# Optimization experiments

Measured on AMD Instinct MI355X. Metric: run time of the kernel, lower is better.

The kernel has to match this reference:

```python
import jax, jax.numpy as jnp
import numpy as np


def _conv(x, w):
    # 'same'-padded NCHW conv, stride 1, no bias (matches nn.Conv2d(..., padding=k//2, bias=False))
    return jax.lax.conv_general_dilated(x, w, (1, 1), 'SAME',
                                        dimension_numbers=('NCHW', 'OIHW', 'NCHW'))


def setup_inputs() -> dict:
    key = jax.random.key(0)
    ks = jax.random.split(key, 11)
    b, C, H, W = 8, 64, 192, 192
    n_classes, n_space = 2, 8
    return {
        'x': jax.random.normal(ks[0], (b, C, H, W), jnp.float32),
        'class_score': jax.random.normal(ks[1], (b, n_classes, H, W), jnp.float32),
        # to_cspace: Conv2d(1, n_space-1, 3, padding=1)
        'W_cspace': jax.random.normal(ks[2], (n_space - 1, 1, 3, 3), jnp.float32) * 0.1,
        # to_xspace: Conv2d(C, C*n_space, 3, padding=1)
        'W_xspace': jax.random.normal(ks[3], (C * n_space, C, 3, 3), jnp.float32) * 0.02,
        # 1x1 convs stored as squeezed vectors (no bias)
        'W_combine_space': jax.random.normal(ks[4], (n_space,), jnp.float32) * 0.3,  # Conv2d(n_space,1,1)
        'W_cvalue': jax.random.normal(ks[5], (n_space,), jnp.float32) * 0.3,        # Conv2d(1,n_space,1)
        'W_attn': jax.random.normal(ks[6], (n_space,), jnp.float32) * 0.3,          # Conv2d(1,n_space,1)
        'W_combine': jax.random.normal(ks[7], (n_space,), jnp.float32) * 0.3,       # Conv2d(n_space,1,1)
        # single_conv: Conv2d(C,C,3) + BatchNorm2d(C) + ReLU
        'W_single': jax.random.normal(ks[8], (C, C, 3, 3), jnp.float32) * 0.02,
        'bn_gamma': jnp.ones((C,), jnp.float32),
        'bn_beta': jnp.zeros((C,), jnp.float32),
    }


def reference(x, class_score, W_cspace, W_xspace, W_combine_space, W_cvalue,
              W_attn, W_combine, W_single, bn_gamma, bn_beta):
    b, C, H, Wd = x.shape
    nc = class_score.shape[1]           # n_classes
    s = W_cvalue.shape[0]               # n_space
    class_prob = jax.nn.sigmoid(class_score)                       # (b, c, H, W)

    # per-class spatial 'spaces'
    space0 = class_prob.reshape(b * nc, 1, H, Wd)                  # (b*c, 1, H, W)
    space = jnp.concatenate([space0, jax.nn.sigmoid(_conv(space0, W_cspace))], axis=1)  # (b*c, s, H, W)
    space_norm = space / jnp.sum(space, axis=(2, 3), keepdims=True)
    space_norm = space_norm.reshape(b, nc, s, H, Wd).transpose(0, 2, 1, 3, 4)  # (b, s, c, H, W)

    # project x into s spaces, then contract over spatial dims (replaces broadcast-mul + double sum)
    xv = _conv(x, W_xspace).reshape(b, s, C, H, Wd)                # (b, s, d, H, W)
    tok = jnp.einsum('bsdhw,bschw->bscd', xv, space_norm)          # (b, s, c, d)
    tok = jnp.einsum('s,bscd->bcd', W_combine_space, tok)          # combine_space 1x1 conv -> (b, c, d)

    # class value / attention (1x1 convs over a singleton channel == broadcast scale)
    cval = tok[:, None] * W_cvalue[None, :, None, None]            # (b, s, c, d)
    attn = class_prob.reshape(b, nc, H * Wd).transpose(0, 2, 1)    # (b, hw, c)
    attn = jax.nn.sigmoid(attn[:, None] * W_attn[None, :, None, None])  # (b, s, hw, c)

    # attention matmul + combine 1x1 conv fused into one contraction (linear ops commute)
    info = jnp.einsum('s,bsnc,bscd->bnd', W_combine, attn, cval)   # (b, hw, d)
    info = info.transpose(0, 2, 1).reshape(b, C, H, Wd)            # (b, d, H, W)

    # single_conv: conv3x3 -> BatchNorm2d (training-mode batch stats, biased var) -> ReLU
    y = _conv(info, W_single)
    mean = jnp.mean(y, axis=(0, 2, 3), keepdims=True)
    var = jnp.var(y, axis=(0, 2, 3), keepdims=True)
    y = jax.nn.relu((y - mean) * jax.lax.rsqrt(var + 1e-5)
                    * bn_gamma[None, :, None, None] + bn_beta[None, :, None, None])
    return x + y
```

## Files before the change

### kernel.cpp

```cpp
#include <hip/hip_runtime.h>
#include <math.h>

#define B   8
#define C   64
#define HH  192
#define WWD 192
#define P   (HH*WWD)
#define NC  2
#define NS  8
#define PP  (194*194)

#define OFF_SPACE 0
#define OFF_SPART 4817408
#define OFF_R     4835840
#define OFF_TOK2  4909568
#define OFF_U     4910592
#define OFF_STP   4919808
#define OFF_SCALE 4956672
#define OFF_SHIFT 4956736
#define WS_FLOATS 4956800

__device__ __forceinline__ float sigm(float x) { return 1.0f / (1.0f + expf(-x)); }

__global__ void k_space(const float* __restrict__ cs, const float* __restrict__ Wc,
                        float* __restrict__ spp, float* __restrict__ Spart) {
    int m = blockIdx.y;
    int bx = blockIdx.x;
    int p = bx * 256 + threadIdx.x;
    int h = p / WWD, w = p - (p / WWD) * WWD;
    float cp[9];
    #pragma unroll
    for (int ky = 0; ky < 3; ky++)
        #pragma unroll
        for (int kx = 0; kx < 3; kx++) {
            int hh = h + ky - 1, ww = w + kx - 1;
            float v = 0.f;
            if ((unsigned)hh < HH && (unsigned)ww < WWD)
                v = sigm(cs[m * P + hh * WWD + ww]);
            cp[ky * 3 + kx] = v;
        }
    float ch[8];
    ch[0] = cp[4];
    #pragma unroll
    for (int j = 0; j < 7; j++) {
        float a = 0.f;
        #pragma unroll
        for (int k = 0; k < 9; k++) a += Wc[j * 9 + k] * cp[k];
        ch[j + 1] = sigm(a);
    }
    #pragma unroll
    for (int q = 0; q < 8; q++)
        spp[(m * 8 + q) * PP + (h + 1) * 194 + (w + 1)] = ch[q];
    __shared__ float red[4][8];
    int lane = threadIdx.x & 63, wave = threadIdx.x >> 6;
    #pragma unroll
    for (int q = 0; q < 8; q++) {
        float v = ch[q];
        for (int off = 32; off > 0; off >>= 1) v += __shfl_down(v, off);
        if (lane == 0) red[wave][q] = v;
    }
    __syncthreads();
    if (threadIdx.x < 8) {
        int q = threadIdx.x;
        Spart[(m * 8 + q) * 144 + bx] = red[0][q] + red[1][q] + red[2][q] + red[3][q];
    }
}

__launch_bounds__(256, 3)
__global__ void k_R2(const float* __restrict__ x, const float* __restrict__ spp,
                     float* __restrict__ R) {
    int ig = blockIdx.x;
    int scz = blockIdx.y;
    int b  = blockIdx.z;
    int sc = scz & 15;
    int half = scz >> 4;
    int s = sc >> 1, c = sc & 1;
    const float* xb = x + (b * C + ig * 8) * P;
    const float* sp = spp + ((b * NC + c) * NS + s) * PP;

    float acc[8][9];
    #pragma unroll
    for (int i = 0; i < 8; i++)
        #pragma unroll
        for (int t = 0; t < 9; t++) acc[i][t] = 0.f;

    for (int it = half * 18; it < half * 18 + 18; it++) {
        int p0 = it * 1024 + threadIdx.x * 4;
        int h = p0 / WWD, w0 = p0 - (p0 / WWD) * WWD;
        float4 xv[8];
        #pragma unroll
        for (int i = 0; i < 8; i++) xv[i] = *(const float4*)(xb + i * P + p0);
        float g[3][6];
        #pragma unroll
        for (int ty = 0; ty < 3; ty++) {
            const float* rp = sp + (h + 2 - ty) * 194 + w0;
            #pragma unroll
            for (int cc = 0; cc < 6; cc++) g[ty][cc] = rp[cc];
        }
        #pragma unroll
        for (int ty = 0; ty < 3; ty++)
            #pragma unroll
            for (int tx = 0; tx < 3; tx++) {
                float g0 = g[ty][2 - tx], g1 = g[ty][3 - tx];
                float g2 = g[ty][4 - tx], g3 = g[ty][5 - tx];
                #pragma unroll
                for (int i = 0; i < 8; i++) {
                    float a = acc[i][ty * 3 + tx];
                    a += xv[i].x * g0; a += xv[i].y * g1;
                    a += xv[i].z * g2; a += xv[i].w * g3;
                    acc[i][ty * 3 + tx] = a;
                }
            }
    }

    __shared__ float red[4][72];
    int lane = threadIdx.x & 63, wave = threadIdx.x >> 6;
    #pragma unroll
    for (int i = 0; i < 8; i++)
        #pragma unroll
        for (int t = 0; t < 9; t++) {
            float v = acc[i][t];
            for (int off = 32; off > 0; off >>= 1) v += __shfl_down(v, off);
            if (lane == 0) red[wave][i * 9 + t] = v;
        }
    __syncthreads();
    if (threadIdx.x < 72) {
        int i = threadIdx.x / 9, t = threadIdx.x - (threadIdx.x / 9) * 9;
        float v = red[0][threadIdx.x] + red[1][threadIdx.x] +
                  red[2][threadIdx.x] + red[3][threadIdx.x];
        atomicAdd(&R[((b * 16 + sc) * 64 + (ig * 8 + i)) * 9 + t], v);
    }
}

__global__ void k_tok2(const float* __restrict__ Wxs, const float* __restrict__ Wcs,
                       const float* __restrict__ R, const float* __restrict__ Spart,
                       float* __restrict__ tok2) {
    int bc = blockIdx.x, s = blockIdx.y;
    int d = threadIdx.x;
    const float* spp = Spart + (bc * 8 + s) * 144;
    float sv = 0.f;
    for (int k = d; k < 144; k += 64) sv += spp[k];
    #pragma unroll
    for (int msk = 32; msk >= 1; msk >>= 1) sv += __shfl_xor(sv, msk);

    const float* Rp = R + ((bc & 1) + ((bc >> 1) * 16 + s * 2)) * 64 * 9;
    const float* Wp = Wxs + (s * C + d) * (C * 9);
    float a = 0.f;
    for (int t = 0; t < C * 9; t++) a += Wp[t] * Rp[t];
    float val = a * Wcs[s] / sv;
    atomicAdd(&tok2[bc * C + d], val);
}

__global__ void k_U(const float* __restrict__ Ws, const float* __restrict__ tok2,
                    float* __restrict__ U) {
    int b = blockIdx.x, m = blockIdx.y, oc = threadIdx.x;
    const float* tp = tok2 + (b * NC + m) * C;
    float u[9];
    #pragma unroll
    for (int t = 0; t < 9; t++) u[t] = 0.f;
    for (int ci = 0; ci < C; ci++) {
        float tv = tp[ci];
        const float* wp = Ws + (oc * C + ci) * 9;
        #pragma unroll
        for (int t = 0; t < 9; t++) u[t] += wp[t] * tv;
    }
    float* up = U + ((b * C + oc) * 2 + m) * 9;
    #pragma unroll
    for (int t = 0; t < 9; t++) up[t] = u[t];
}

__device__ __forceinline__ void stage_g(const float* __restrict__ cs, int b, int ty0, int tx0,
                                        const float* __restrict__ Wcval,
                                        const float* __restrict__ Wattn,
                                        const float* __restrict__ Wcomb,
                                        float* h0, float* h1) {
    float wa[8], wt[8];
    #pragma unroll
    for (int s = 0; s < 8; s++) { wa[s] = Wcomb[s] * Wcval[s]; wt[s] = Wattn[s]; }
    for (int idx = threadIdx.x; idx < 34 * 34; idx += 256) {
        int i = idx / 34, j = idx - (idx / 34) * 34;
        int gy = ty0 - 1 + i, gx = tx0 - 1 + j;
        float a0 = 0.f, a1 = 0.f;
        if ((unsigned)gy < HH && (unsigned)gx < WWD) {
            int p = gy * WWD + gx;
            float c0 = sigm(cs[(b * NC + 0) * P + p]);
            float c1 = sigm(cs[(b * NC + 1) * P + p]);
            #pragma unroll
            for (int s = 0; s < 8; s++) {
                a0 += wa[s] * sigm(c0 * wt[s]);
                a1 += wa[s] * sigm(c1 * wt[s]);
            }
        }
        h0[i * 35 + j] = a0; h1[i * 35 + j] = a1;
    }
}

__launch_bounds__(256)
__global__ void k_cs(const float* __restrict__ cs, const float* __restrict__ U,
                     const float* __restrict__ Wcval, const float* __restrict__ Wattn,
                     const float* __restrict__ Wcomb, float* __restrict__ STp) {
    int tile = blockIdx.x, ocg = blockIdx.y, b = blockIdx.z;
    int ty0 = (tile / 6) * 32, tx0 = (tile % 6) * 32;
    __shared__ float h0[34 * 35], h1[34 * 35];
    stage_g(cs, b, ty0, tx0, Wcval, Wattn, Wcomb, h0, h1);
    __syncthreads();

    int w = __builtin_amdgcn_readfirstlane(threadIdx.x >> 6);
    int lane = threadIdx.x & 63;
    int oc0 = ocg * 8 + w * 2;
    float u0[2][9], u1[2][9];
    #pragma unroll
    for (int j = 0; j < 2; j++) {
        const float* up = U + ((b * C + oc0 + j) * 2) * 9;
        #pragma unroll
        for (int t = 0; t < 9; t++) { u0[j][t] = up[t]; u1[j][t] = up[9 + t]; }
    }
    float s1[2] = {0.f, 0.f}, s2[2] = {0.f, 0.f};
    for (int it = 0; it < 4; it++) {
        int row = it * 8 + (lane >> 3);
        int c0 = (lane & 7) * 4;
        float g0v[3][6], g1v[3][6];
        #pragma unroll
        for (int dy = 0; dy < 3; dy++)
            #pragma unroll
            for (int dx = 0; dx < 6; dx++) {
                g0v[dy][dx] = h0[(row + dy) * 35 + c0 + dx];
                g1v[dy][dx] = h1[(row + dy) * 35 + c0 + dx];
            }
        #pragma unroll
        for (int j = 0; j < 2; j++)
            #pragma unroll
            for (int px = 0; px < 4; px++) {
                float y = 0.f;
                #pragma unroll
                for (int ky = 0; ky < 3; ky++)
                    #pragma unroll
                    for (int kx = 0; kx < 3; kx++) {
                        y += u0[j][ky * 3 + kx] * g0v[ky][px + kx];
                        y += u1[j][ky * 3 + kx] * g1v[ky][px + kx];
                    }
                s1[j] += y; s2[j] += y * y;
            }
    }
    #pragma unroll
    for (int j = 0; j < 2; j++) {
        float a = s1[j], q = s2[j];
        for (int off = 32; off > 0; off >>= 1) { a += __shfl_down(a, off); q += __shfl_down(q, off); }
        if (lane == 0) {
            int slot = b * 36 + tile;
            STp[(oc0 + j) * 288 + slot] = a;
            STp[64 * 288 + (oc0 + j) * 288 + slot] = q;
        }
    }
}

__global__ void k_bnfin(const float* __restrict__ STp, const float* __restrict__ gamma,
                        const float* __restrict__ beta, float* __restrict__ scale,
                        float* __restrict__ shift) {
    int oc = threadIdx.x;
    double s = 0.0, s2 = 0.0;
    for (int k = 0; k < 288; k++) {
        s  += (double)STp[oc * 288 + k];
        s2 += (double)STp[64 * 288 + oc * 288 + k];
    }
    double n = (double)(B * P);
    double mean = s / n;
    double var = s2 / n - mean * mean;
    float sc = gamma[oc] * rsqrtf((float)var + 1e-5f);
    scale[oc] = sc;
    shift[oc] = beta[oc] - (float)mean * sc;
}

__launch_bounds__(256)
__global__ void k_fin2(const float* __restrict__ cs, const float* __restrict__ U,
                       const float* __restrict__ Wcval, const float* __restrict__ Wattn,
                       const float* __restrict__ Wcomb, const float* __restrict__ x,
                       const float* __restrict__ scale, const float* __restrict__ shift,
                       float* __restrict__ out) {
    int tile = blockIdx.x, ocg = blockIdx.y, b = blockIdx.z;
    int ty0 = (tile / 6) * 32, tx0 = (tile % 6) * 32;
    __shared__ float h0[34 * 35], h1[34 * 35];
    stage_g(cs, b, ty0, tx0, Wcval, Wattn, Wcomb, h0, h1);
    __syncthreads();

    int w = __builtin_amdgcn_readfirstlane(threadIdx.x >> 6);
    int lane = threadIdx.x & 63;
    int oc0 = ocg * 8 + w * 2;
    float u0[2][9], u1[2][9], sc[2], sh[2];
    #pragma unroll
    for (int j = 0; j < 2; j++) {
        const float* up = U + ((b * C + oc0 + j) * 2) * 9;
        #pragma unroll
        for (int t = 0; t < 9; t++) { u0[j][t] = up[t]; u1[j][t] = up[9 + t]; }
        sc[j] = scale[oc0 + j]; sh[j] = shift[oc0 + j];
    }
    for (int it = 0; it < 4; it++) {
        int row = it * 8 + (lane >> 3);
        int c0 = (lane & 7) * 4;
        float g0v[3][6], g1v[3][6];
        #pragma unroll
        for (int dy = 0; dy < 3; dy++)
            #pragma unroll
            for (int dx = 0; dx < 6; dx++) {
                g0v[dy][dx] = h0[(row + dy) * 35 + c0 + dx];
                g1v[dy][dx] = h1[(row + dy) * 35 + c0 + dx];
            }
        #pragma unroll
        for (int j = 0; j < 2; j++) {
            float y4[4];
            #pragma unroll
            for (int px = 0; px < 4; px++) {
                float y = 0.f;
                #pragma unroll
                for (int ky = 0; ky < 3; ky++)
                    #pragma unroll
                    for (int kx = 0; kx < 3; kx++) {
                        y += u0[j][ky * 3 + kx] * g0v[ky][px + kx];
                        y += u1[j][ky * 3 + kx] * g1v[ky][px + kx];
                    }
                y4[px] = y;
            }
            int ga = (b * C + oc0 + j) * P + (ty0 + row) * WWD + tx0 + c0;
            float4 xv = *(const float4*)(x + ga);
            float4 ov;
            ov.x = fmaxf(y4[0] * sc[j] + sh[j], 0.f) + xv.x;
            ov.y = fmaxf(y4[1] * sc[j] + sh[j], 0.f) + xv.y;
            ov.z = fmaxf(y4[2] * sc[j] + sh[j], 0.f) + xv.z;
            ov.w = fmaxf(y4[3] * sc[j] + sh[j], 0.f) + xv.w;
            *(float4*)(out + ga) = ov;
        }
    }
}

extern "C" void kernel_launch(void* const* d_in, const int* in_sizes, int n_in,
                              void* d_out, int out_size, void* d_ws, size_t ws_size,
                              hipStream_t stream) {
    const float* x     = (const float*)d_in[0];
    const float* cs    = (const float*)d_in[1];
    const float* Wc    = (const float*)d_in[2];
    const float* Wxs   = (const float*)d_in[3];
    const float* Wcsp  = (const float*)d_in[4];
    const float* Wcval = (const float*)d_in[5];
    const float* Wattn = (const float*)d_in[6];
    const float* Wcomb = (const float*)d_in[7];
    const float* Wsing = (const float*)d_in[8];
    const float* gamma = (const float*)d_in[9];
    const float* beta  = (const float*)d_in[10];
    float* ws  = (float*)d_ws;
    float* out = (float*)d_out;

    float* spp   = ws + OFF_SPACE;
    float* Spart = ws + OFF_SPART;
    float* R     = ws + OFF_R;
    float* tok2  = ws + OFF_TOK2;
    float* U     = ws + OFF_U;
    float* STp   = ws + OFF_STP;
    float* scale = ws + OFF_SCALE;
    float* shift = ws + OFF_SHIFT;

    hipMemsetAsync(ws, 0, (size_t)(OFF_TOK2 + 1024) * sizeof(float), stream);

    k_space<<<dim3(144, 16), 256, 0, stream>>>(cs, Wc, spp, Spart);
    k_R2   <<<dim3(8, 32, 8), 256, 0, stream>>>(x, spp, R);
    k_tok2 <<<dim3(16, 8), 64, 0, stream>>>(Wxs, Wcsp, R, Spart, tok2);
    k_U    <<<dim3(8, 2), 64, 0, stream>>>(Wsing, tok2, U);
    k_cs   <<<dim3(36, 8, 8), 256, 0, stream>>>(cs, U, Wcval, Wattn, Wcomb, STp);
    k_bnfin<<<1, 64, 0, stream>>>(STp, gamma, beta, scale, shift);
    k_fin2 <<<dim3(36, 8, 8), 256, 0, stream>>>(cs, U, Wcval, Wattn, Wcomb, x, scale, shift, out);
}
```

Measured before the change: 448.7 us.

## Precompute attention gate map once and transpose Wxspace for coalesced token reduction

Adds a kernel that computes the per-pixel gated attention value (sigmoid mixture over 8 spaces) once into a workspace map. Before this, k_cs and k_fin2 recomputed it for every output-channel group and halo pixel, costing 18 sigmoids per pixel repeatedly. Also transposes W_xspace so the k_tok2 dot products read coalesced across threads, vectorizes the stencil loads in k_R2, and transposes the BN partial-stats layout. The new buffers reuse the start of the workspace, which the space buffer occupies. This is safe only because that buffer is dead after k_R2, and it adds extra launches plus global-memory traffic.

```diff
diff --git a/kernel.cpp b/kernel.cpp
--- a/kernel.cpp
+++ b/kernel.cpp
@@ -11,6 +11,8 @@
 #define PP  (194*194)
 
 #define OFF_SPACE 0
+#define OFF_WT    0
+#define OFF_GM    294912
 #define OFF_SPART 4817408
 #define OFF_R     4835840
 #define OFF_TOK2  4909568
@@ -94,8 +96,11 @@
         #pragma unroll
         for (int ty = 0; ty < 3; ty++) {
             const float* rp = sp + (h + 2 - ty) * 194 + w0;
-            #pragma unroll
-            for (int cc = 0; cc < 6; cc++) g[ty][cc] = rp[cc];
+            float4 ga; float2 gb;
+            __builtin_memcpy(&ga, rp, 16);
+            __builtin_memcpy(&gb, rp + 4, 8);
+            g[ty][0] = ga.x; g[ty][1] = ga.y; g[ty][2] = ga.z;
+            g[ty][3] = ga.w; g[ty][4] = gb.x; g[ty][5] = gb.y;
         }
         #pragma unroll
         for (int ty = 0; ty < 3; ty++)
@@ -132,7 +137,29 @@
     }
 }
 
-__global__ void k_tok2(const float* __restrict__ Wxs, const float* __restrict__ Wcs,
+__global__ void k_wt(const float* __restrict__ Wxs, float* __restrict__ Wt) {
+    int t = blockIdx.x;
+    int s = blockIdx.y;
+    int d = threadIdx.x;
+    Wt[(s * 576 + t) * 64 + d] = Wxs[(s * 64 + d) * 576 + t];
+}
+
+__global__ void k_g(const float* __restrict__ cs, const float* __restrict__ Wcval,
+                    const float* __restrict__ Wattn, const float* __restrict__ Wcomb,
+                    float* __restrict__ gmap) {
+    int m = blockIdx.y;
+    int p = blockIdx.x * 256 + threadIdx.x;
+    float wa[8], wt[8];
+    #pragma unroll
+    for (int s = 0; s < 8; s++) { wa[s] = Wcomb[s] * Wcval[s]; wt[s] = Wattn[s]; }
+    float cp = sigm(cs[m * P + p]);
+    float a = 0.f;
+    #pragma unroll
+    for (int s = 0; s < 8; s++) a += wa[s] * sigm(cp * wt[s]);
+    gmap[m * P + p] = a;
+}
+
+__global__ void k_tok2(const float* __restrict__ Wt, const float* __restrict__ Wcs,
                        const float* __restrict__ R, const float* __restrict__ Spart,
                        float* __restrict__ tok2) {
     int bc = blockIdx.x, s = blockIdx.y;
@@ -143,10 +170,11 @@
     #pragma unroll
     for (int msk = 32; msk >= 1; msk >>= 1) sv += __shfl_xor(sv, msk);
 
-    const float* Rp = R + ((bc & 1) + ((bc >> 1) * 16 + s * 2)) * 64 * 9;
-    const float* Wp = Wxs + (s * C + d) * (C * 9);
+    const float* Rp = R + ((bc & 1) + ((bc >> 1) * 16 + s * 2)) * 576;
+    const float* Wp = Wt + s * 576 * 64 + d;
     float a = 0.f;
-    for (int t = 0; t < C * 9; t++) a += Wp[t] * Rp[t];
+    #pragma unroll 4
+    for (int t = 0; t < 576; t++) a += Wp[t * 64] * Rp[t];
     float val = a * Wcs[s] / sv;
     atomicAdd(&tok2[bc * C + d], val);
 }
@@ -169,40 +197,29 @@
     for (int t = 0; t < 9; t++) up[t] = u[t];
 }
 
-__device__ __forceinline__ void stage_g(const float* __restrict__ cs, int b, int ty0, int tx0,
-                                        const float* __restrict__ Wcval,
-                                        const float* __restrict__ Wattn,
-                                        const float* __restrict__ Wcomb,
+__device__ __forceinline__ void stage_g(const float* __restrict__ gmap, int b, int ty0, int tx0,
                                         float* h0, float* h1) {
-    float wa[8], wt[8];
-    #pragma unroll
-    for (int s = 0; s < 8; s++) { wa[s] = Wcomb[s] * Wcval[s]; wt[s] = Wattn[s]; }
+    const float* g0p = gmap + (b * NC + 0) * P;
+    const float* g1p = gmap + (b * NC + 1) * P;
     for (int idx = threadIdx.x; idx < 34 * 34; idx += 256) {
         int i = idx / 34, j = idx - (idx / 34) * 34;
         int gy = ty0 - 1 + i, gx = tx0 - 1 + j;
         float a0 = 0.f, a1 = 0.f;
         if ((unsigned)gy < HH && (unsigned)gx < WWD) {
             int p = gy * WWD + gx;
-            float c0 = sigm(cs[(b * NC + 0) * P + p]);
-            float c1 = sigm(cs[(b * NC + 1) * P + p]);
-            #pragma unroll
-            for (int s = 0; s < 8; s++) {
-                a0 += wa[s] * sigm(c0 * wt[s]);
-                a1 += wa[s] * sigm(c1 * wt[s]);
-            }
+            a0 = g0p[p]; a1 = g1p[p];
         }
         h0[i * 35 + j] = a0; h1[i * 35 + j] = a1;
     }
 }
 
 __launch_bounds__(256)
-__global__ void k_cs(const float* __restrict__ cs, const float* __restrict__ U,
-                     const float* __restrict__ Wcval, const float* __restrict__ Wattn,
-                     const float* __restrict__ Wcomb, float* __restrict__ STp) {
+__global__ void k_cs(const float* __restrict__ gmap, const float* __restrict__ U,
+                     float* __restrict__ STp) {
     int tile = blockIdx.x, ocg = blockIdx.y, b = blockIdx.z;
     int ty0 = (tile / 6) * 32, tx0 = (tile % 6) * 32;
     __shared__ float h0[34 * 35], h1[34 * 35];
-    stage_g(cs, b, ty0, tx0, Wcval, Wattn, Wcomb, h0, h1);
+    stage_g(gmap, b, ty0, tx0, h0, h1);
     __syncthreads();
 
     int w = __builtin_amdgcn_readfirstlane(threadIdx.x >> 6);
@@ -248,8 +265,8 @@
         for (int off = 32; off > 0; off >>= 1) { a += __shfl_down(a, off); q += __shfl_down(q, off); }
         if (lane == 0) {
             int slot = b * 36 + tile;
-            STp[(oc0 + j) * 288 + slot] = a;
-            STp[64 * 288 + (oc0 + j) * 288 + slot] = q;
+            STp[slot * 64 + (oc0 + j)] = a;
+            STp[288 * 64 + slot * 64 + (oc0 + j)] = q;
         }
     }
 }
@@ -260,8 +277,8 @@
     int oc = threadIdx.x;
     double s = 0.0, s2 = 0.0;
     for (int k = 0; k < 288; k++) {
-        s  += (double)STp[oc * 288 + k];
-        s2 += (double)STp[64 * 288 + oc * 288 + k];
+        s  += (double)STp[k * 64 + oc];
+        s2 += (double)STp[288 * 64 + k * 64 + oc];
     }
     double n = (double)(B * P);
     double mean = s / n;
@@ -272,15 +289,14 @@
 }
 
 __launch_bounds__(256)
-__global__ void k_fin2(const float* __restrict__ cs, const float* __restrict__ U,
-                       const float* __restrict__ Wcval, const float* __restrict__ Wattn,
-                       const float* __restrict__ Wcomb, const float* __restrict__ x,
+__global__ void k_fin2(const float* __restrict__ gmap, const float* __restrict__ U,
+                       const float* __restrict__ x,
                        const float* __restrict__ scale, const float* __restrict__ shift,
                        float* __restrict__ out) {
     int tile = blockIdx.x, ocg = blockIdx.y, b = blockIdx.z;
     int ty0 = (tile / 6) * 32, tx0 = (tile % 6) * 32;
     __shared__ float h0[34 * 35], h1[34 * 35];
-    stage_g(cs, b, ty0, tx0, Wcval, Wattn, Wcomb, h0, h1);
+    stage_g(gmap, b, ty0, tx0, h0, h1);
     __syncthreads();
 
     int w = __builtin_amdgcn_readfirstlane(threadIdx.x >> 6);
@@ -350,6 +366,8 @@
     float* out = (float*)d_out;
 
     float* spp   = ws + OFF_SPACE;
+    float* Wt    = ws + OFF_WT;
+    float* gmap  = ws + OFF_GM;
     float* Spart = ws + OFF_SPART;
     float* R     = ws + OFF_R;
     float* tok2  = ws + OFF_TOK2;
@@ -362,9 +380,11 @@
 
     k_space<<<dim3(144, 16), 256, 0, stream>>>(cs, Wc, spp, Spart);
     k_R2   <<<dim3(8, 32, 8), 256, 0, stream>>>(x, spp, R);
-    k_tok2 <<<dim3(16, 8), 64, 0, stream>>>(Wxs, Wcsp, R, Spart, tok2);
+    k_wt   <<<dim3(576, 8), 64, 0, stream>>>(Wxs, Wt);
+    k_g    <<<dim3(144, 16), 256, 0, stream>>>(cs, Wcval, Wattn, Wcomb, gmap);
+    k_tok2 <<<dim3(16, 8), 64, 0, stream>>>(Wt, Wcsp, R, Spart, tok2);
     k_U    <<<dim3(8, 2), 64, 0, stream>>>(Wsing, tok2, U);
-    k_cs   <<<dim3(36, 8, 8), 256, 0, stream>>>(cs, U, Wcval, Wattn, Wcomb, STp);
+    k_cs   <<<dim3(36, 8, 8), 256, 0, stream>>>(gmap, U, STp);
     k_bnfin<<<1, 64, 0, stream>>>(STp, gamma, beta, scale, shift);
-    k_fin2 <<<dim3(36, 8, 8), 256, 0, stream>>>(cs, U, Wcval, Wattn, Wcomb, x, scale, shift, out);
-}
+    k_fin2 <<<dim3(36, 8, 8), 256, 0, stream>>>(gmap, U, x, scale, shift, out);
+}
```

Result: faster. 426.6 us (-4.9%).
